# Kernel tuning notes

Hardware: AMD Instinct MI355X
Metric: run time of the kernel (lower is better)

## Reference

```python
import jax, jax.numpy as jnp
import numpy as np
import math

B, S, A, E = 64, 8, 128, 256
H = 4
D = E // H  # head_dim = 64


def setup_inputs() -> dict:
    key = jax.random.key(0)
    ks = jax.random.split(key, 10)
    scale = 1.0 / math.sqrt(E)
    return {
        "predicate_emb": jax.random.normal(ks[0], (B, S, A, 1, E), jnp.float32),
        "constant_embs": jax.random.normal(ks[1], (B, S, A, 2, E), jnp.float32),
        "Wq": jax.random.normal(ks[2], (E, E), jnp.float32) * scale,
        "bq": jax.random.normal(ks[3], (E,), jnp.float32) * scale,
        "Wk": jax.random.normal(ks[4], (E, E), jnp.float32) * scale,
        "bk": jax.random.normal(ks[5], (E,), jnp.float32) * scale,
        "Wv": jax.random.normal(ks[6], (E, E), jnp.float32) * scale,
        "bv": jax.random.normal(ks[7], (E,), jnp.float32) * scale,
        "Wo": jax.random.normal(ks[8], (E, E), jnp.float32) * scale,
        "bo": jax.random.normal(ks[9], (E,), jnp.float32) * scale,
    }


def reference(predicate_emb, constant_embs, Wq, bq, Wk, bk, Wv, bv, Wo, bo):
    # dropout_rate = 0.0 -> dropout is identity
    p = predicate_emb[..., 0, :]                       # [B,S,A,E]  (squeeze(3))
    Q = p @ Wq.T + bq                                  # [B,S,A,E]
    K = constant_embs @ Wk.T + bk                      # [B,S,A,2,E]
    V = constant_embs @ Wv.T + bv                      # [B,S,A,2,E]

    Qh = Q.reshape(B, S, A, H, D)                      # [B,S,A,H,D]
    Kh = K.reshape(B, S, A, 2, H, D)                   # [B,S,A,2,H,D]
    Vh = V.reshape(B, S, A, 2, H, D)

    inv_sqrt_d = 1.0 / math.sqrt(D)
    # scores over the 2 keys per (atom, head)
    scores = jnp.einsum('bsahd,bsakhd->bsahk', Qh, Kh) * inv_sqrt_d  # [B,S,A,H,2]
    attn = jax.nn.softmax(scores, axis=-1)                            # [B,S,A,H,2]
    ws = jnp.einsum('bsahk,bsakhd->bsahd', attn, Vh)                  # [B,S,A,H,D]

    concat = ws.reshape(B, S, A, E)
    return concat @ Wo.T + bo                           # [B,S,A,E]
```

## Files before the change

### kernel.cpp

```cpp
#include <hip/hip_runtime.h>

#define LSTR 264

typedef short short4v __attribute__((ext_vector_type(4)));
typedef short short8v __attribute__((ext_vector_type(8)));
typedef float f32x4 __attribute__((ext_vector_type(4)));

#define MFMA(a, b, c) __builtin_amdgcn_mfma_f32_16x16x32_bf16((a), (b), (c), 0, 0, 0)

__device__ __forceinline__ short f2bf(float f) {
  unsigned u = __float_as_uint(f);
  unsigned r = u + 0x7fffu + ((u >> 16) & 1u);
  return (short)(r >> 16);
}

__device__ __forceinline__ short4v f2bf4(float4 v) {
  short4v s;
  s.x = f2bf(v.x); s.y = f2bf(v.y); s.z = f2bf(v.z); s.w = f2bf(v.w);
  return s;
}


__global__ __launch_bounds__(256) void prep1_kernel(
    const float* __restrict__ Wv, const float* __restrict__ Wo,
    const float* __restrict__ bv, const float* __restrict__ bo,
    short* __restrict__ pvo, float* __restrict__ bvo) {
  __shared__ float srow[256];
  __shared__ float red[256];
  const int n = blockIdx.x, k = threadIdx.x;
  const float wov = Wo[n * 256 + k];
  srow[k] = wov;
  red[k] = wov * bv[k];
  __syncthreads();
  float acc = 0.f;
#pragma unroll 16
  for (int j = 0; j < 256; ++j) acc += srow[j] * Wv[j * 256 + k];
  const int h = n >> 6, nt = (n >> 4) & 3, col = n & 15;
  const int ks = k >> 5, quad = (k >> 3) & 3, j8 = k & 7;
  pvo[h * 16384 + (ks * 4 + nt) * 512 + (quad * 16 + col) * 8 + j8] = f2bf(acc);
  for (int s = 128; s > 0; s >>= 1) {
    if (k < s) red[k] += red[k + s];
    __syncthreads();
  }
  if (k == 0) bvo[n] = red[0] + bo[n];
}

__global__ __launch_bounds__(256) void pack_kernel(
    const float* __restrict__ Wq, const float* __restrict__ Wk,
    const float* __restrict__ Wv, const float* __restrict__ Wo,
    short* __restrict__ pq, short* __restrict__ pk,
    short* __restrict__ pv, short* __restrict__ po) {
  const int g = blockIdx.x * 256 + threadIdx.x;
  const int n = g >> 5;
  const int c8 = g & 31;
  const int h = n >> 6, nt = (n >> 4) & 3, col = n & 15;
  const int ks = c8 >> 2, quad = c8 & 3;
  const int src = n * 256 + c8 * 8;
  const int dst = h * 16384 + (ks * 4 + nt) * 512 + (quad * 16 + col) * 8;
  const float4* q4 = (const float4*)(Wq + src);
  const float4* k4 = (const float4*)(Wk + src);
  const float4* v4 = (const float4*)(Wv + src);
  const float4* o4 = (const float4*)(Wo + src);
  float4 qa = q4[0], qb = q4[1], ka = k4[0], kb = k4[1];
  float4 va = v4[0], vb = v4[1], oa = o4[0], ob = o4[1];
  *(short4v*)(pq + dst) = f2bf4(qa); *(short4v*)(pq + dst + 4) = f2bf4(qb);
  *(short4v*)(pk + dst) = f2bf4(ka); *(short4v*)(pk + dst + 4) = f2bf4(kb);
  *(short4v*)(pv + dst) = f2bf4(va); *(short4v*)(pv + dst + 4) = f2bf4(vb);
  *(short4v*)(po + dst) = f2bf4(oa); *(short4v*)(po + dst + 4) = f2bf4(ob);
}

__device__ __forceinline__ void gemm1(const short* A, const short* __restrict__ wb,
                                      int col, int quad, f32x4 acc[2][4]) {
  const short* a0p = A + col * LSTR + quad * 8;
  const short* a1p = a0p + 16 * LSTR;
  short8v a0c = *(const short8v*)a0p;
  short8v a1c = *(const short8v*)a1p;
  short8v b0 = *(const short8v*)(wb);
  short8v b1 = *(const short8v*)(wb + 512);
#pragma unroll
  for (int ks = 0; ks < 8; ++ks) {
    const int kn = (ks + 1) & 7;
    short8v a0n = *(const short8v*)(a0p + kn * 32);
    short8v a1n = *(const short8v*)(a1p + kn * 32);
#pragma unroll
    for (int nt = 0; nt < 4; ++nt) {
      const int f = ks * 4 + nt;
      short8v bn = *(const short8v*)(wb + ((f + 2) & 31) * 512);
      acc[0][nt] = MFMA(a0c, b0, acc[0][nt]);
      acc[1][nt] = MFMA(a1c, b0, acc[1][nt]);
      b0 = b1; b1 = bn;
    }
    a0c = a0n; a1c = a1n;
  }
}

__global__ __launch_bounds__(256, 3) void fused_kernel(
    const float* __restrict__ pred, const float* __restrict__ cemb,
    const short* __restrict__ pq, const short* __restrict__ pk,
    const short* __restrict__ pv, const short* __restrict__ po,
    const short* __restrict__ pvo, const float* __restrict__ bq,
    const float* __restrict__ bvo, float* __restrict__ out) {
  __shared__ __align__(16) short bufP[32 * LSTR];
  __shared__ __align__(16) short bufD[32 * LSTR];
  __shared__ __align__(16) short bufC1[32 * LSTR];
  const int tid = threadIdx.x;
  const size_t t0 = (size_t)blockIdx.x * 32;

  {
    const int r = tid >> 3;
    const int c0 = tid & 7;
    const float4* prow = (const float4*)(pred + (t0 + r) * 256);
    const float4* crow = (const float4*)(cemb + (t0 + r) * 512);
    float4 pv_[8], av[8], bw[8];
#pragma unroll
    for (int i = 0; i < 8; ++i) pv_[i] = prow[c0 + 8 * i];
#pragma unroll
    for (int i = 0; i < 8; ++i) av[i] = crow[c0 + 8 * i];
#pragma unroll
    for (int i = 0; i < 8; ++i) bw[i] = crow[64 + c0 + 8 * i];
    short* pd = bufP + r * LSTR;
    short* dd = bufD + r * LSTR;
    short* cd = bufC1 + r * LSTR;
#pragma unroll
    for (int i = 0; i < 8; ++i) {
      const int j = c0 + 8 * i;
      *(short4v*)(pd + 4 * j) = f2bf4(pv_[i]);
      float4 d4 = make_float4(av[i].x - bw[i].x, av[i].y - bw[i].y,
                              av[i].z - bw[i].z, av[i].w - bw[i].w);
      *(short4v*)(dd + 4 * j) = f2bf4(d4);
      *(short4v*)(cd + 4 * j) = f2bf4(bw[i]);
    }
  }
  __syncthreads();

  const int lane = tid & 63;
  const int w = tid >> 6;
  const int col = lane & 15;
  const int quad = lane >> 4;
  const int nbase = w * 64;
  const int woff = w * 16384 + lane * 8;

  float bqv[4];
#pragma unroll
  for (int nt = 0; nt < 4; ++nt) bqv[nt] = bq[nbase + nt * 16 + col];

  f32x4 accQ[2][4] = {};
  gemm1(bufP, pq + woff, col, quad, accQ);
  f32x4 accK[2][4] = {};
  gemm1(bufD, pk + woff, col, quad, accK);

  float g[2][4];
#pragma unroll
  for (int ms = 0; ms < 2; ++ms) {
#pragma unroll
    for (int r = 0; r < 4; ++r) {
      float zz = 0.f;
#pragma unroll
      for (int nt = 0; nt < 4; ++nt)
        zz += (accQ[ms][nt][r] + bqv[nt]) * accK[ms][nt][r];
      zz += __shfl_xor(zz, 1);
      zz += __shfl_xor(zz, 2);
      zz += __shfl_xor(zz, 4);
      zz += __shfl_xor(zz, 8);
      g[ms][r] = 1.f / (1.f + __expf(-0.125f * zz));
    }
  }

  f32x4 accV[2][4] = {};
  gemm1(bufD, pv + woff, col, quad, accV);

  __syncthreads();
#pragma unroll
  for (int ms = 0; ms < 2; ++ms)
#pragma unroll
    for (int nt = 0; nt < 4; ++nt)
#pragma unroll
      for (int r = 0; r < 4; ++r)
        bufP[(ms * 16 + quad * 4 + r) * LSTR + nbase + nt * 16 + col] =
            f2bf(g[ms][r] * accV[ms][nt][r]);
  __syncthreads();

  f32x4 accO[2][4] = {};
  gemm1(bufC1, pvo + woff, col, quad, accO);
  gemm1(bufP, po + woff, col, quad, accO);

  float bov[4];
#pragma unroll
  for (int nt = 0; nt < 4; ++nt) bov[nt] = bvo[nbase + nt * 16 + col];

#pragma unroll
  for (int ms = 0; ms < 2; ++ms)
#pragma unroll
    for (int nt = 0; nt < 4; ++nt)
#pragma unroll
      for (int r = 0; r < 4; ++r)
        out[(t0 + ms * 16 + quad * 4 + r) * 256 + nbase + nt * 16 + col] =
            accO[ms][nt][r] + bov[nt];
}

extern "C" void kernel_launch(void* const* d_in, const int* in_sizes, int n_in,
                              void* d_out, int out_size, void* d_ws, size_t ws_size,
                              hipStream_t stream) {
  const float* pred = (const float*)d_in[0];
  const float* cemb = (const float*)d_in[1];
  const float* Wq = (const float*)d_in[2];
  const float* bq = (const float*)d_in[3];
  const float* Wk = (const float*)d_in[4];
  const float* Wv = (const float*)d_in[6];
  const float* bv = (const float*)d_in[7];
  const float* Wo = (const float*)d_in[8];
  const float* bo = (const float*)d_in[9];
  float* out = (float*)d_out;

  short* pq = (short*)d_ws;
  short* pk = pq + 65536;
  short* pv = pk + 65536;
  short* po = pv + 65536;
  short* pvo = po + 65536;
  float* bvo = (float*)(pvo + 65536);

  prep1_kernel<<<256, 256, 0, stream>>>(Wv, Wo, bv, bo, pvo, bvo);
  pack_kernel<<<32, 256, 0, stream>>>(Wq, Wk, Wv, Wo, pq, pk, pv, po);
  fused_kernel<<<2048, 256, 0, stream>>>(pred, cemb, pq, pk, pv, po, pvo, bq, bvo, out);
}
```

Measured before the change: 337.1 us.

## Stage constant embeddings via direct global-to-LDS loads and fuse GEMM passes

The constant embeddings now go straight from global memory into a swizzled fp32 LDS buffer through global_load_lds. The key difference and the second constant are computed and packed to bf16 on the fly inside the GEMM loops. The Q, K and V GEMMs are fused into one pass that shares the A-fragment loads, and the two output GEMMs into another with separate accumulators. The predicate tile is stored in MFMA-fragment order so fragment reads are conflict-free. This removes the register round-trip and the separate conversion stage. In exchange it uses a larger fp32 LDS footprint and higher register pressure, so occupancy is lowered to 2 blocks per CU, and the fp32-to-bf16 conversion is now repeated inside the loops.

Result: slower. 348.9 us (+3.5%).

```diff
diff --git a/kernel.cpp b/kernel.cpp
--- a/kernel.cpp
+++ b/kernel.cpp
@@ -1,6 +1,4 @@
 #include <hip/hip_runtime.h>
-
-#define LSTR 264
 
 typedef short short4v __attribute__((ext_vector_type(4)));
 typedef short short8v __attribute__((ext_vector_type(8)));
@@ -18,6 +16,19 @@
   short4v s;
   s.x = f2bf(v.x); s.y = f2bf(v.y); s.z = f2bf(v.z); s.w = f2bf(v.w);
   return s;
+}
+
+__device__ __forceinline__ short8v pack8(float4 a, float4 b) {
+  short8v s;
+  s[0] = f2bf(a.x); s[1] = f2bf(a.y); s[2] = f2bf(a.z); s[3] = f2bf(a.w);
+  s[4] = f2bf(b.x); s[5] = f2bf(b.y); s[6] = f2bf(b.z); s[7] = f2bf(b.w);
+  return s;
+}
+
+__device__ __forceinline__ void gload_lds16(const void* g, void* l) {
+  __builtin_amdgcn_global_load_lds(
+      (const __attribute__((address_space(1))) unsigned int*)g,
+      (__attribute__((address_space(3))) unsigned int*)l, 16, 0, 0);
 }
 
 
@@ -69,133 +80,200 @@
   *(short4v*)(po + dst) = f2bf4(oa); *(short4v*)(po + dst + 4) = f2bf4(ob);
 }
 
-__device__ __forceinline__ void gemm1(const short* A, const short* __restrict__ wb,
-                                      int col, int quad, f32x4 acc[2][4]) {
-  const short* a0p = A + col * LSTR + quad * 8;
-  const short* a1p = a0p + 16 * LSTR;
-  short8v a0c = *(const short8v*)a0p;
-  short8v a1c = *(const short8v*)a1p;
-  short8v b0 = *(const short8v*)(wb);
-  short8v b1 = *(const short8v*)(wb + 512);
+__device__ __forceinline__ void passA(const short* bufP, const float* bufC,
+                                      const short* __restrict__ wq,
+                                      const short* __restrict__ wk,
+                                      const short* __restrict__ wv, int lane,
+                                      f32x4 accQ[2][4], f32x4 accK[2][4],
+                                      f32x4 accV[2][4]) {
+  const int rlo = lane & 15, quad = lane >> 4, r7 = lane & 7;
+  short8v qb0 = *(const short8v*)(wq);
+  short8v qb1 = *(const short8v*)(wq + 512);
+  short8v kb0 = *(const short8v*)(wk);
+  short8v kb1 = *(const short8v*)(wk + 512);
+  short8v vb0 = *(const short8v*)(wv);
+  short8v vb1 = *(const short8v*)(wv + 512);
 #pragma unroll
   for (int ks = 0; ks < 8; ++ks) {
-    const int kn = (ks + 1) & 7;
-    short8v a0n = *(const short8v*)(a0p + kn * 32);
-    short8v a1n = *(const short8v*)(a1p + kn * 32);
+    short8v pf[2], df[2];
+#pragma unroll
+    for (int ms = 0; ms < 2; ++ms) {
+      pf[ms] = *(const short8v*)(bufP + ((ks * 2 + ms) * 64 + lane) * 8);
+      const int row = ms * 16 + rlo;
+      const int cb = ks * 8 + quad * 2;
+      const float* rb = bufC + (row << 9);
+      float4 c0a = *(const float4*)(rb + (((cb) ^ r7) << 2));
+      float4 c0b = *(const float4*)(rb + (((cb + 1) ^ r7) << 2));
+      float4 c1a = *(const float4*)(rb + (((64 + cb) ^ r7) << 2));
+      float4 c1b = *(const float4*)(rb + (((64 + cb + 1) ^ r7) << 2));
+      float4 d0 = make_float4(c0a.x - c1a.x, c0a.y - c1a.y, c0a.z - c1a.z, c0a.w - c1a.w);
+      float4 d1 = make_float4(c0b.x - c1b.x, c0b.y - c1b.y, c0b.z - c1b.z, c0b.w - c1b.w);
+      df[ms] = pack8(d0, d1);
+    }
 #pragma unroll
     for (int nt = 0; nt < 4; ++nt) {
       const int f = ks * 4 + nt;
-      short8v bn = *(const short8v*)(wb + ((f + 2) & 31) * 512);
-      acc[0][nt] = MFMA(a0c, b0, acc[0][nt]);
-      acc[1][nt] = MFMA(a1c, b0, acc[1][nt]);
-      b0 = b1; b1 = bn;
-    }
-    a0c = a0n; a1c = a1n;
-  }
-}
-
-__global__ __launch_bounds__(256, 3) void fused_kernel(
+      short8v qn = *(const short8v*)(wq + ((f + 2) & 31) * 512);
+      short8v kn = *(const short8v*)(wk + ((f + 2) & 31) * 512);
+      short8v vn = *(const short8v*)(wv + ((f + 2) & 31) * 512);
+      accQ[0][nt] = MFMA(pf[0], qb0, accQ[0][nt]);
+      accQ[1][nt] = MFMA(pf[1], qb0, accQ[1][nt]);
+      accK[0][nt] = MFMA(df[0], kb0, accK[0][nt]);
+      accK[1][nt] = MFMA(df[1], kb0, accK[1][nt]);
+      accV[0][nt] = MFMA(df[0], vb0, accV[0][nt]);
+      accV[1][nt] = MFMA(df[1], vb0, accV[1][nt]);
+      qb0 = qb1; qb1 = qn;
+      kb0 = kb1; kb1 = kn;
+      vb0 = vb1; vb1 = vn;
+    }
+  }
+}
+
+__device__ __forceinline__ void passB(const short* bufG, const float* bufC,
+                                      const short* __restrict__ wvo,
+                                      const short* __restrict__ wo, int lane,
+                                      f32x4 acc1[2][4], f32x4 acc2[2][4]) {
+  const int rlo = lane & 15, quad = lane >> 4, r7 = lane & 7;
+  short8v v0 = *(const short8v*)(wvo);
+  short8v v1 = *(const short8v*)(wvo + 512);
+  short8v o0 = *(const short8v*)(wo);
+  short8v o1 = *(const short8v*)(wo + 512);
+#pragma unroll
+  for (int ks = 0; ks < 8; ++ks) {
+    short8v cf[2], gf[2];
+#pragma unroll
+    for (int ms = 0; ms < 2; ++ms) {
+      gf[ms] = *(const short8v*)(bufG + ((ks * 2 + ms) * 64 + lane) * 8);
+      const int row = ms * 16 + rlo;
+      const int cb = ks * 8 + quad * 2;
+      const float* rb = bufC + (row << 9);
+      float4 c1a = *(const float4*)(rb + (((64 + cb) ^ r7) << 2));
+      float4 c1b = *(const float4*)(rb + (((64 + cb + 1) ^ r7) << 2));
+      cf[ms] = pack8(c1a, c1b);
+    }
+#pragma unroll
+    for (int nt = 0; nt < 4; ++nt) {
+      const int f = ks * 4 + nt;
+      short8v vn = *(const short8v*)(wvo + ((f + 2) & 31) * 512);
+      short8v on = *(const short8v*)(wo + ((f + 2) & 31) * 512);
+      acc1[0][nt] = MFMA(cf[0], v0, acc1[0][nt]);
+      acc1[1][nt] = MFMA(cf[1], v0, acc1[1][nt]);
+      acc2[0][nt] = MFMA(gf[0], o0, acc2[0][nt]);
+      acc2[1][nt] = MFMA(gf[1], o0, acc2[1][nt]);
+      v0 = v1; v1 = vn;
+      o0 = o1; o1 = on;
+    }
+  }
+}
+
+__global__ __launch_bounds__(256, 2) void fused_kernel(
     const float* __restrict__ pred, const float* __restrict__ cemb,
     const short* __restrict__ pq, const short* __restrict__ pk,
     const short* __restrict__ pv, const short* __restrict__ po,
     const short* __restrict__ pvo, const float* __restrict__ bq,
     const float* __restrict__ bvo, float* __restrict__ out) {
-  __shared__ __align__(16) short bufP[32 * LSTR];
-  __shared__ __align__(16) short bufD[32 * LSTR];
-  __shared__ __align__(16) short bufC1[32 * LSTR];
+  __shared__ __align__(16) float bufC[32 * 512];
+  __shared__ __align__(16) short bufP[8192];
   const int tid = threadIdx.x;
   const size_t t0 = (size_t)blockIdx.x * 32;
-
-  {
-    const int r = tid >> 3;
-    const int c0 = tid & 7;
-    const float4* prow = (const float4*)(pred + (t0 + r) * 256);
-    const float4* crow = (const float4*)(cemb + (t0 + r) * 512);
-    float4 pv_[8], av[8], bw[8];
-#pragma unroll
-    for (int i = 0; i < 8; ++i) pv_[i] = prow[c0 + 8 * i];
-#pragma unroll
-    for (int i = 0; i < 8; ++i) av[i] = crow[c0 + 8 * i];
-#pragma unroll
-    for (int i = 0; i < 8; ++i) bw[i] = crow[64 + c0 + 8 * i];
-    short* pd = bufP + r * LSTR;
-    short* dd = bufD + r * LSTR;
-    short* cd = bufC1 + r * LSTR;
-#pragma unroll
-    for (int i = 0; i < 8; ++i) {
-      const int j = c0 + 8 * i;
-      *(short4v*)(pd + 4 * j) = f2bf4(pv_[i]);
-      float4 d4 = make_float4(av[i].x - bw[i].x, av[i].y - bw[i].y,
-                              av[i].z - bw[i].z, av[i].w - bw[i].w);
-      *(short4v*)(dd + 4 * j) = f2bf4(d4);
-      *(short4v*)(cd + 4 * j) = f2bf4(bw[i]);
-    }
-  }
-  __syncthreads();
-
   const int lane = tid & 63;
   const int w = tid >> 6;
+
+  const int r = tid >> 3;
+  const int c8 = tid & 7;
+  const float4* prow = (const float4*)(pred + (t0 + r) * 256);
+  float4 pv_[8];
+#pragma unroll
+  for (int i = 0; i < 8; ++i) pv_[i] = prow[c8 + 8 * i];
+
+  {
+#pragma unroll
+    for (int rr = 0; rr < 8; ++rr) {
+      const int row = w * 8 + rr;
+      const int r7 = row & 7;
+      const float* gb = cemb + (t0 + row) * 512;
+      float* lb = bufC + row * 512;
+      const int lsw = (lane ^ r7) << 2;
+      gload_lds16(gb + lsw, lb);
+      gload_lds16(gb + 256 + lsw, lb + 256);
+    }
+  }
+
   const int col = lane & 15;
   const int quad = lane >> 4;
   const int nbase = w * 64;
   const int woff = w * 16384 + lane * 8;
 
-  float bqv[4];
+  float bqv[4], bov[4];
 #pragma unroll
   for (int nt = 0; nt < 4; ++nt) bqv[nt] = bq[nbase + nt * 16 + col];
+#pragma unroll
+  for (int nt = 0; nt < 4; ++nt) bov[nt] = bvo[nbase + nt * 16 + col];
+
+  {
+    const int ms = r >> 4;
+    const int r15 = r & 15;
+#pragma unroll
+    for (int i = 0; i < 8; ++i) {
+      const int k0 = 4 * (c8 + 8 * i);
+      const int ks = k0 >> 5, q2 = (k0 >> 3) & 3, j = k0 & 7;
+      *(short4v*)(bufP + ((ks * 2 + ms) * 64 + q2 * 16 + r15) * 8 + j) =
+          f2bf4(pv_[i]);
+    }
+  }
+  asm volatile("s_waitcnt vmcnt(0)");
+  __syncthreads();
 
   f32x4 accQ[2][4] = {};
-  gemm1(bufP, pq + woff, col, quad, accQ);
   f32x4 accK[2][4] = {};
-  gemm1(bufD, pk + woff, col, quad, accK);
+  f32x4 accV[2][4] = {};
+  passA(bufP, bufC, pq + woff, pk + woff, pv + woff, lane, accQ, accK, accV);
 
   float g[2][4];
 #pragma unroll
   for (int ms = 0; ms < 2; ++ms) {
 #pragma unroll
-    for (int r = 0; r < 4; ++r) {
+    for (int rr = 0; rr < 4; ++rr) {
       float zz = 0.f;
 #pragma unroll
       for (int nt = 0; nt < 4; ++nt)
-        zz += (accQ[ms][nt][r] + bqv[nt]) * accK[ms][nt][r];
+        zz += (accQ[ms][nt][rr] + bqv[nt]) * accK[ms][nt][rr];
       zz += __shfl_xor(zz, 1);
       zz += __shfl_xor(zz, 2);
       zz += __shfl_xor(zz, 4);
       zz += __shfl_xor(zz, 8);
-      g[ms][r] = 1.f / (1.f + __expf(-0.125f * zz));
-    }
-  }
-
-  f32x4 accV[2][4] = {};
-  gemm1(bufD, pv + woff, col, quad, accV);
+      g[ms][rr] = 1.f / (1.f + __expf(-0.125f * zz));
+    }
+  }
 
   __syncthreads();
+
 #pragma unroll
   for (int ms = 0; ms < 2; ++ms)
 #pragma unroll
+    for (int nt = 0; nt < 4; ++nt) {
+      const int ks2 = w * 2 + (nt >> 1);
+      const int quad2 = ((nt & 1) * 2 + (col >> 3)) & 3;
+      const int j = col & 7;
+#pragma unroll
+      for (int rr = 0; rr < 4; ++rr)
+        bufP[((ks2 * 2 + ms) * 64 + quad2 * 16 + quad * 4 + rr) * 8 + j] =
+            f2bf(g[ms][rr] * accV[ms][nt][rr]);
+    }
+  __syncthreads();
+
+  f32x4 accO1[2][4] = {};
+  f32x4 accO2[2][4] = {};
+  passB(bufP, bufC, pvo + woff, po + woff, lane, accO1, accO2);
+
+#pragma unroll
+  for (int ms = 0; ms < 2; ++ms)
+#pragma unroll
     for (int nt = 0; nt < 4; ++nt)
 #pragma unroll
-      for (int r = 0; r < 4; ++r)
-        bufP[(ms * 16 + quad * 4 + r) * LSTR + nbase + nt * 16 + col] =
-            f2bf(g[ms][r] * accV[ms][nt][r]);
-  __syncthreads();
-
-  f32x4 accO[2][4] = {};
-  gemm1(bufC1, pvo + woff, col, quad, accO);
-  gemm1(bufP, po + woff, col, quad, accO);
-
-  float bov[4];
-#pragma unroll
-  for (int nt = 0; nt < 4; ++nt) bov[nt] = bvo[nbase + nt * 16 + col];
-
-#pragma unroll
-  for (int ms = 0; ms < 2; ++ms)
-#pragma unroll
-    for (int nt = 0; nt < 4; ++nt)
-#pragma unroll
-      for (int r = 0; r < 4; ++r)
-        out[(t0 + ms * 16 + quad * 4 + r) * 256 + nbase + nt * 16 + col] =
-            accO[ms][nt][r] + bov[nt];
+      for (int rr = 0; rr < 4; ++rr)
+        out[(t0 + ms * 16 + quad * 4 + rr) * 256 + nbase + nt * 16 + col] =
+            accO1[ms][nt][rr] + accO2[ms][nt][rr] + bov[nt];
 }
 
 extern "C" void kernel_launch(void* const* d_in, const int* in_sizes, int n_in,
```

## Retile fused attention kernel to 64-row blocks with swizzled LDS and merged prep

Applied to the files above, without the earlier changes.

Merges the two weight-preparation kernels into one launch, saving a launch. The fused kernel now handles 64 tokens per 512-thread block, with each pair of waves splitting a head's 64 output columns. Q·K partial dot products are combined across the pair through a small shared buffer. Shared tiles use an XOR swizzle instead of padding, and the c1 tile is reloaded from global memory late to save LDS. The aim is better weight reuse per block and fewer bank conflicts, at the cost of an extra barrier and a second read of cemb.

Result: faster. 319.8 us (-5.1%).

```diff
diff --git a/kernel.cpp b/kernel.cpp
--- a/kernel.cpp
+++ b/kernel.cpp
@@ -1,6 +1,4 @@
 #include <hip/hip_runtime.h>
-
-#define LSTR 264
 
 typedef short short4v __attribute__((ext_vector_type(4)));
 typedef short short8v __attribute__((ext_vector_type(8)));
@@ -21,181 +19,255 @@
 }
 
 
-__global__ __launch_bounds__(256) void prep1_kernel(
+
+__global__ __launch_bounds__(256) void prep_kernel(
+    const float* __restrict__ Wq, const float* __restrict__ Wk,
     const float* __restrict__ Wv, const float* __restrict__ Wo,
     const float* __restrict__ bv, const float* __restrict__ bo,
+    short* __restrict__ pq, short* __restrict__ pk,
+    short* __restrict__ pv, short* __restrict__ po,
     short* __restrict__ pvo, float* __restrict__ bvo) {
   __shared__ float srow[256];
   __shared__ float red[256];
-  const int n = blockIdx.x, k = threadIdx.x;
-  const float wov = Wo[n * 256 + k];
-  srow[k] = wov;
-  red[k] = wov * bv[k];
-  __syncthreads();
-  float acc = 0.f;
+  if (blockIdx.x < 256) {
+    const int n = blockIdx.x, k = threadIdx.x;
+    const float wov = Wo[n * 256 + k];
+    srow[k] = wov;
+    red[k] = wov * bv[k];
+    __syncthreads();
+    float acc = 0.f;
 #pragma unroll 16
-  for (int j = 0; j < 256; ++j) acc += srow[j] * Wv[j * 256 + k];
-  const int h = n >> 6, nt = (n >> 4) & 3, col = n & 15;
-  const int ks = k >> 5, quad = (k >> 3) & 3, j8 = k & 7;
-  pvo[h * 16384 + (ks * 4 + nt) * 512 + (quad * 16 + col) * 8 + j8] = f2bf(acc);
-  for (int s = 128; s > 0; s >>= 1) {
-    if (k < s) red[k] += red[k + s];
-    __syncthreads();
-  }
-  if (k == 0) bvo[n] = red[0] + bo[n];
-}
-
-__global__ __launch_bounds__(256) void pack_kernel(
-    const float* __restrict__ Wq, const float* __restrict__ Wk,
-    const float* __restrict__ Wv, const float* __restrict__ Wo,
-    short* __restrict__ pq, short* __restrict__ pk,
-    short* __restrict__ pv, short* __restrict__ po) {
-  const int g = blockIdx.x * 256 + threadIdx.x;
-  const int n = g >> 5;
-  const int c8 = g & 31;
-  const int h = n >> 6, nt = (n >> 4) & 3, col = n & 15;
-  const int ks = c8 >> 2, quad = c8 & 3;
-  const int src = n * 256 + c8 * 8;
-  const int dst = h * 16384 + (ks * 4 + nt) * 512 + (quad * 16 + col) * 8;
-  const float4* q4 = (const float4*)(Wq + src);
-  const float4* k4 = (const float4*)(Wk + src);
-  const float4* v4 = (const float4*)(Wv + src);
-  const float4* o4 = (const float4*)(Wo + src);
-  float4 qa = q4[0], qb = q4[1], ka = k4[0], kb = k4[1];
-  float4 va = v4[0], vb = v4[1], oa = o4[0], ob = o4[1];
-  *(short4v*)(pq + dst) = f2bf4(qa); *(short4v*)(pq + dst + 4) = f2bf4(qb);
-  *(short4v*)(pk + dst) = f2bf4(ka); *(short4v*)(pk + dst + 4) = f2bf4(kb);
-  *(short4v*)(pv + dst) = f2bf4(va); *(short4v*)(pv + dst + 4) = f2bf4(vb);
-  *(short4v*)(po + dst) = f2bf4(oa); *(short4v*)(po + dst + 4) = f2bf4(ob);
-}
-
-__device__ __forceinline__ void gemm1(const short* A, const short* __restrict__ wb,
-                                      int col, int quad, f32x4 acc[2][4]) {
-  const short* a0p = A + col * LSTR + quad * 8;
-  const short* a1p = a0p + 16 * LSTR;
-  short8v a0c = *(const short8v*)a0p;
-  short8v a1c = *(const short8v*)a1p;
-  short8v b0 = *(const short8v*)(wb);
-  short8v b1 = *(const short8v*)(wb + 512);
-#pragma unroll
-  for (int ks = 0; ks < 8; ++ks) {
-    const int kn = (ks + 1) & 7;
-    short8v a0n = *(const short8v*)(a0p + kn * 32);
-    short8v a1n = *(const short8v*)(a1p + kn * 32);
-#pragma unroll
-    for (int nt = 0; nt < 4; ++nt) {
-      const int f = ks * 4 + nt;
-      short8v bn = *(const short8v*)(wb + ((f + 2) & 31) * 512);
-      acc[0][nt] = MFMA(a0c, b0, acc[0][nt]);
-      acc[1][nt] = MFMA(a1c, b0, acc[1][nt]);
-      b0 = b1; b1 = bn;
-    }
-    a0c = a0n; a1c = a1n;
-  }
-}
-
-__global__ __launch_bounds__(256, 3) void fused_kernel(
+    for (int j = 0; j < 256; ++j) acc += srow[j] * Wv[j * 256 + k];
+    const int h = n >> 6, nt = (n >> 4) & 3, col = n & 15;
+    const int ks = k >> 5, quad = (k >> 3) & 3, j8 = k & 7;
+    pvo[h * 16384 + (ks * 4 + nt) * 512 + (quad * 16 + col) * 8 + j8] = f2bf(acc);
+    for (int s = 128; s > 0; s >>= 1) {
+      if (k < s) red[k] += red[k + s];
+      __syncthreads();
+    }
+    if (k == 0) bvo[n] = red[0] + bo[n];
+  } else {
+    const int g = (blockIdx.x - 256) * 256 + threadIdx.x;
+    const int n = g >> 5;
+    const int c8 = g & 31;
+    const int h = n >> 6, nt = (n >> 4) & 3, col = n & 15;
+    const int ks = c8 >> 2, quad = c8 & 3;
+    const int src = n * 256 + c8 * 8;
+    const int dst = h * 16384 + (ks * 4 + nt) * 512 + (quad * 16 + col) * 8;
+    const float4* q4 = (const float4*)(Wq + src);
+    const float4* k4 = (const float4*)(Wk + src);
+    const float4* v4 = (const float4*)(Wv + src);
+    const float4* o4 = (const float4*)(Wo + src);
+    float4 qa = q4[0], qb = q4[1], ka = k4[0], kb = k4[1];
+    float4 va = v4[0], vb = v4[1], oa = o4[0], ob = o4[1];
+    *(short4v*)(pq + dst) = f2bf4(qa); *(short4v*)(pq + dst + 4) = f2bf4(qb);
+    *(short4v*)(pk + dst) = f2bf4(ka); *(short4v*)(pk + dst + 4) = f2bf4(kb);
+    *(short4v*)(pv + dst) = f2bf4(va); *(short4v*)(pv + dst + 4) = f2bf4(vb);
+    *(short4v*)(po + dst) = f2bf4(oa); *(short4v*)(po + dst + 4) = f2bf4(ob);
+  }
+}
+
+__global__ __launch_bounds__(512, 4) void fused_kernel(
     const float* __restrict__ pred, const float* __restrict__ cemb,
     const short* __restrict__ pq, const short* __restrict__ pk,
     const short* __restrict__ pv, const short* __restrict__ po,
     const short* __restrict__ pvo, const float* __restrict__ bq,
     const float* __restrict__ bvo, float* __restrict__ out) {
-  __shared__ __align__(16) short bufP[32 * LSTR];
-  __shared__ __align__(16) short bufD[32 * LSTR];
-  __shared__ __align__(16) short bufC1[32 * LSTR];
+  __shared__ __align__(16) short X[16384];
+  __shared__ __align__(16) short Y[16384];
+  __shared__ float zbuf[512];
   const int tid = threadIdx.x;
-  const size_t t0 = (size_t)blockIdx.x * 32;
-
-  {
-    const int r = tid >> 3;
-    const int c0 = tid & 7;
-    const float4* prow = (const float4*)(pred + (t0 + r) * 256);
-    const float4* crow = (const float4*)(cemb + (t0 + r) * 512);
-    float4 pv_[8], av[8], bw[8];
-#pragma unroll
-    for (int i = 0; i < 8; ++i) pv_[i] = prow[c0 + 8 * i];
-#pragma unroll
-    for (int i = 0; i < 8; ++i) av[i] = crow[c0 + 8 * i];
-#pragma unroll
-    for (int i = 0; i < 8; ++i) bw[i] = crow[64 + c0 + 8 * i];
-    short* pd = bufP + r * LSTR;
-    short* dd = bufD + r * LSTR;
-    short* cd = bufC1 + r * LSTR;
-#pragma unroll
-    for (int i = 0; i < 8; ++i) {
-      const int j = c0 + 8 * i;
-      *(short4v*)(pd + 4 * j) = f2bf4(pv_[i]);
-      float4 d4 = make_float4(av[i].x - bw[i].x, av[i].y - bw[i].y,
-                              av[i].z - bw[i].z, av[i].w - bw[i].w);
-      *(short4v*)(dd + 4 * j) = f2bf4(d4);
-      *(short4v*)(cd + 4 * j) = f2bf4(bw[i]);
-    }
-  }
-  __syncthreads();
-
   const int lane = tid & 63;
   const int w = tid >> 6;
+  const int h = w & 3;
+  const int nhalf = w >> 2;
   const int col = lane & 15;
   const int quad = lane >> 4;
-  const int nbase = w * 64;
-  const int woff = w * 16384 + lane * 8;
-
-  float bqv[4];
-#pragma unroll
-  for (int nt = 0; nt < 4; ++nt) bqv[nt] = bq[nbase + nt * 16 + col];
-
-  f32x4 accQ[2][4] = {};
-  gemm1(bufP, pq + woff, col, quad, accQ);
-  f32x4 accK[2][4] = {};
-  gemm1(bufD, pk + woff, col, quad, accK);
-
-  float g[2][4];
-#pragma unroll
-  for (int ms = 0; ms < 2; ++ms) {
-#pragma unroll
-    for (int r = 0; r < 4; ++r) {
-      float zz = 0.f;
-#pragma unroll
-      for (int nt = 0; nt < 4; ++nt)
-        zz += (accQ[ms][nt][r] + bqv[nt]) * accK[ms][nt][r];
+  const int x7 = col & 7;
+  const size_t t0 = (size_t)blockIdx.x * 64;
+  const int rA = tid >> 3;
+  const int c8 = tid & 7;
+  const int nbase = h * 64 + nhalf * 32;
+  const short* wqp = pq + h * 16384 + nhalf * 1024 + lane * 8;
+  const short* wkp = pk + h * 16384 + nhalf * 1024 + lane * 8;
+  const short* wvp = pv + h * 16384 + nhalf * 1024 + lane * 8;
+  const short* wop = po + h * 16384 + nhalf * 1024 + lane * 8;
+  const short* wvop = pvo + h * 16384 + nhalf * 1024 + lane * 8;
+
+  float bqv[2], bov[2];
+#pragma unroll
+  for (int n2 = 0; n2 < 2; ++n2) bqv[n2] = bq[nbase + n2 * 16 + col];
+#pragma unroll
+  for (int n2 = 0; n2 < 2; ++n2) bov[n2] = bvo[nbase + n2 * 16 + col];
+
+  const float4* prow = (const float4*)(pred + (t0 + rA) * 256);
+  const float4* crow = (const float4*)(cemb + (t0 + rA) * 512);
+  const int rx = rA & 7;
+
+  {
+    float4 pvv[8], c0v[8], c1v[8];
+#pragma unroll
+    for (int i = 0; i < 8; ++i) pvv[i] = prow[c8 + 8 * i];
+#pragma unroll
+    for (int i = 0; i < 8; ++i) c0v[i] = crow[c8 + 8 * i];
+#pragma unroll
+    for (int i = 0; i < 8; ++i) c1v[i] = crow[64 + c8 + 8 * i];
+#pragma unroll
+    for (int i = 0; i < 8; ++i) {
+      const int h2 = c8 + 8 * i;
+      const int off = rA * 256 + ((((h2 >> 1) ^ rx)) << 3) + (h2 & 1) * 4;
+      *(short4v*)(X + off) = f2bf4(pvv[i]);
+      float4 d4 = make_float4(c0v[i].x - c1v[i].x, c0v[i].y - c1v[i].y,
+                              c0v[i].z - c1v[i].z, c0v[i].w - c1v[i].w);
+      *(short4v*)(Y + off) = f2bf4(d4);
+    }
+  }
+  __syncthreads();
+
+  f32x4 accQ[4][2] = {};
+  f32x4 accK[4][2] = {};
+  {
+    short8v qb0 = *(const short8v*)(wqp);
+    short8v qb1 = *(const short8v*)(wqp + 512);
+    short8v kb0 = *(const short8v*)(wkp);
+    short8v kb1 = *(const short8v*)(wkp + 512);
+#pragma unroll
+    for (int ks = 0; ks < 8; ++ks) {
+      const int kk = ((ks + 1) & 7) * 2048;
+      short8v qn0 = *(const short8v*)(wqp + kk);
+      short8v qn1 = *(const short8v*)(wqp + kk + 512);
+      short8v kn0 = *(const short8v*)(wkp + kk);
+      short8v kn1 = *(const short8v*)(wkp + kk + 512);
+      const int ao = (((ks * 4 + quad) ^ x7) << 3);
+#pragma unroll
+      for (int ms = 0; ms < 4; ++ms) {
+        const int ro = (ms * 16 + col) * 256 + ao;
+        short8v ap = *(const short8v*)(X + ro);
+        short8v ad = *(const short8v*)(Y + ro);
+        accQ[ms][0] = MFMA(ap, qb0, accQ[ms][0]);
+        accQ[ms][1] = MFMA(ap, qb1, accQ[ms][1]);
+        accK[ms][0] = MFMA(ad, kb0, accK[ms][0]);
+        accK[ms][1] = MFMA(ad, kb1, accK[ms][1]);
+      }
+      qb0 = qn0; qb1 = qn1; kb0 = kn0; kb1 = kn1;
+    }
+  }
+
+  float g[4][4];
+#pragma unroll
+  for (int ms = 0; ms < 4; ++ms) {
+#pragma unroll
+    for (int rr = 0; rr < 4; ++rr) {
+      float zz = (accQ[ms][0][rr] + bqv[0]) * accK[ms][0][rr] +
+                 (accQ[ms][1][rr] + bqv[1]) * accK[ms][1][rr];
       zz += __shfl_xor(zz, 1);
       zz += __shfl_xor(zz, 2);
       zz += __shfl_xor(zz, 4);
       zz += __shfl_xor(zz, 8);
-      g[ms][r] = 1.f / (1.f + __expf(-0.125f * zz));
-    }
-  }
-
-  f32x4 accV[2][4] = {};
-  gemm1(bufD, pv + woff, col, quad, accV);
-
-  __syncthreads();
-#pragma unroll
-  for (int ms = 0; ms < 2; ++ms)
-#pragma unroll
-    for (int nt = 0; nt < 4; ++nt)
-#pragma unroll
-      for (int r = 0; r < 4; ++r)
-        bufP[(ms * 16 + quad * 4 + r) * LSTR + nbase + nt * 16 + col] =
-            f2bf(g[ms][r] * accV[ms][nt][r]);
-  __syncthreads();
-
-  f32x4 accO[2][4] = {};
-  gemm1(bufC1, pvo + woff, col, quad, accO);
-  gemm1(bufP, po + woff, col, quad, accO);
-
-  float bov[4];
-#pragma unroll
-  for (int nt = 0; nt < 4; ++nt) bov[nt] = bvo[nbase + nt * 16 + col];
-
-#pragma unroll
-  for (int ms = 0; ms < 2; ++ms)
-#pragma unroll
-    for (int nt = 0; nt < 4; ++nt)
-#pragma unroll
-      for (int r = 0; r < 4; ++r)
-        out[(t0 + ms * 16 + quad * 4 + r) * 256 + nbase + nt * 16 + col] =
-            accO[ms][nt][r] + bov[nt];
+      g[ms][rr] = zz;
+    }
+  }
+  if ((lane & 15) == 0) {
+#pragma unroll
+    for (int ms = 0; ms < 4; ++ms)
+#pragma unroll
+      for (int rr = 0; rr < 4; ++rr)
+        zbuf[h * 128 + nhalf * 64 + ms * 16 + quad * 4 + rr] = g[ms][rr];
+  }
+  __syncthreads();
+#pragma unroll
+  for (int ms = 0; ms < 4; ++ms)
+#pragma unroll
+    for (int rr = 0; rr < 4; ++rr) {
+      const int m = ms * 16 + quad * 4 + rr;
+      const float zt = zbuf[h * 128 + m] + zbuf[h * 128 + 64 + m];
+      g[ms][rr] = 1.f / (1.f + __expf(-0.125f * zt));
+    }
+
+  float4 c1r[8];
+#pragma unroll
+  for (int i = 0; i < 8; ++i) c1r[i] = crow[64 + c8 + 8 * i];
+
+  f32x4 accV[4][2] = {};
+  {
+    short8v vb0 = *(const short8v*)(wvp);
+    short8v vb1 = *(const short8v*)(wvp + 512);
+#pragma unroll
+    for (int ks = 0; ks < 8; ++ks) {
+      const int kk = ((ks + 1) & 7) * 2048;
+      short8v vn0 = *(const short8v*)(wvp + kk);
+      short8v vn1 = *(const short8v*)(wvp + kk + 512);
+      const int ao = (((ks * 4 + quad) ^ x7) << 3);
+#pragma unroll
+      for (int ms = 0; ms < 4; ++ms) {
+        short8v ad = *(const short8v*)(Y + (ms * 16 + col) * 256 + ao);
+        accV[ms][0] = MFMA(ad, vb0, accV[ms][0]);
+        accV[ms][1] = MFMA(ad, vb1, accV[ms][1]);
+      }
+      vb0 = vn0; vb1 = vn1;
+    }
+  }
+  __syncthreads();
+
+#pragma unroll
+  for (int ms = 0; ms < 4; ++ms)
+#pragma unroll
+    for (int n2 = 0; n2 < 2; ++n2) {
+      const int ch = h * 8 + nhalf * 4 + n2 * 2 + (col >> 3);
+      const int j = col & 7;
+#pragma unroll
+      for (int rr = 0; rr < 4; ++rr) {
+        const int row = ms * 16 + quad * 4 + rr;
+        X[row * 256 + ((ch ^ (row & 7)) << 3) + j] =
+            f2bf(g[ms][rr] * accV[ms][n2][rr]);
+      }
+    }
+#pragma unroll
+  for (int i = 0; i < 8; ++i) {
+    const int h2 = c8 + 8 * i;
+    const int off = rA * 256 + ((((h2 >> 1) ^ rx)) << 3) + (h2 & 1) * 4;
+    *(short4v*)(Y + off) = f2bf4(c1r[i]);
+  }
+  __syncthreads();
+
+  f32x4 accO[4][2] = {};
+  {
+    short8v vb0 = *(const short8v*)(wvop);
+    short8v vb1 = *(const short8v*)(wvop + 512);
+    short8v ob0 = *(const short8v*)(wop);
+    short8v ob1 = *(const short8v*)(wop + 512);
+#pragma unroll
+    for (int ks = 0; ks < 8; ++ks) {
+      const int kk = ((ks + 1) & 7) * 2048;
+      short8v vn0 = *(const short8v*)(wvop + kk);
+      short8v vn1 = *(const short8v*)(wvop + kk + 512);
+      short8v on0 = *(const short8v*)(wop + kk);
+      short8v on1 = *(const short8v*)(wop + kk + 512);
+      const int ao = (((ks * 4 + quad) ^ x7) << 3);
+#pragma unroll
+      for (int ms = 0; ms < 4; ++ms) {
+        short8v ac = *(const short8v*)(Y + (ms * 16 + col) * 256 + ao);
+        accO[ms][0] = MFMA(ac, vb0, accO[ms][0]);
+        accO[ms][1] = MFMA(ac, vb1, accO[ms][1]);
+      }
+#pragma unroll
+      for (int ms = 0; ms < 4; ++ms) {
+        short8v ag = *(const short8v*)(X + (ms * 16 + col) * 256 + ao);
+        accO[ms][0] = MFMA(ag, ob0, accO[ms][0]);
+        accO[ms][1] = MFMA(ag, ob1, accO[ms][1]);
+      }
+      vb0 = vn0; vb1 = vn1; ob0 = on0; ob1 = on1;
+    }
+  }
+
+#pragma unroll
+  for (int ms = 0; ms < 4; ++ms)
+#pragma unroll
+    for (int n2 = 0; n2 < 2; ++n2)
+#pragma unroll
+      for (int rr = 0; rr < 4; ++rr)
+        out[(t0 + ms * 16 + quad * 4 + rr) * 256 + nbase + n2 * 16 + col] =
+            accO[ms][n2][rr] + bov[n2];
 }
 
 extern "C" void kernel_launch(void* const* d_in, const int* in_sizes, int n_in,
@@ -219,7 +291,6 @@
   short* pvo = po + 65536;
   float* bvo = (float*)(pvo + 65536);
 
-  prep1_kernel<<<256, 256, 0, stream>>>(Wv, Wo, bv, bo, pvo, bvo);
-  pack_kernel<<<32, 256, 0, stream>>>(Wq, Wk, Wv, Wo, pq, pk, pv, po);
-  fused_kernel<<<2048, 256, 0, stream>>>(pred, cemb, pq, pk, pv, po, pvo, bq, bvo, out);
-}
+  prep_kernel<<<288, 256, 0, stream>>>(Wq, Wk, Wv, Wo, bv, bo, pq, pk, pv, po, pvo, bvo);
+  fused_kernel<<<1024, 512, 0, stream>>>(pred, cemb, pq, pk, pv, po, pvo, bq, bvo, out);
+}
```
